# Kernel tuning notes

Measured on AMD Instinct MI355X. Metric: run time of the kernel, lower is better.

The kernel has to match this reference:

```python
import jax, jax.numpy as jnp
import numpy as np
import math

D_MODEL = 1024
N_HEAD = 16
D_HEAD = D_MODEL // N_HEAD
INIT_SIZE = 1200  # RelativeSinusoidalPositionalEmbedding init_size
SCALE = 1.0       # scale=False in __init__


def _rel_pos_embed(L, d_head):
    """Replicates RelativeSinusoidalPositionalEmbedding: table over positions
    [-601, 600] (num=init_size+1=1201 rows), padding row 0 zeroed, then gather
    rows for positions arange(-L/2, L/2) + origin_shift (origin_shift=601)."""
    num = INIT_SIZE + 1                      # 1201
    half = d_head // 2
    freq = jnp.exp(jnp.arange(half, dtype=jnp.float32) * (-math.log(10000.0) / (half - 1)))
    pos_vals = jnp.arange(-num // 2, num // 2, dtype=jnp.float32)   # -601..599 -> 1201 vals
    ang = pos_vals[:, None] * freq[None, :]
    table = jnp.concatenate([jnp.sin(ang), jnp.cos(ang)], axis=1)   # [num, d_head]
    table = table.at[0].set(0.0)             # padding_idx = 0
    origin_shift = num // 2 + 1              # 601
    idx = jnp.arange(-(L // 2), L // 2) + origin_shift   # L even -> L indices
    return table[idx]                        # [L, d_head]


def setup_inputs() -> dict:
    key = jax.random.key(0)
    k1, k2, k3, k4, k5 = jax.random.split(key, 5)
    B, L = 4, 1024
    embed = jax.random.normal(k1, (B, L, D_MODEL), dtype=jnp.float32)
    umask = jnp.ones((B, L), dtype=jnp.int32)                       # 1 = valid utterance
    qmask = jax.random.randint(k2, (B, L), 0, 2).astype(jnp.int64)  # speaker ids {0,1}
    W_qkv = jax.random.normal(k3, (D_MODEL, 4 * D_MODEL), dtype=jnp.float32) * 0.02
    W_pos = jax.random.normal(k4, (D_HEAD, 3 * D_MODEL), dtype=jnp.float32) * 0.02
    W_fc  = jax.random.normal(k5, (D_MODEL, D_MODEL), dtype=jnp.float32) * 0.02
    return {"embed": embed, "umask": umask, "qmask": qmask,
            "W_qkv": W_qkv, "W_pos": W_pos, "W_fc": W_fc}


def reference(embed, umask, qmask, W_qkv, W_pos, W_fc):
    B, L, d = embed.shape
    H, dh = N_HEAD, d // N_HEAD

    # qkv projection and head split
    q, k1, k2, v = jnp.split(embed @ W_qkv, 4, axis=-1)             # each [B, L, d]
    q  = q.reshape(B, L, H, dh).transpose(0, 2, 1, 3)               # [B, H, L, dh]
    k1 = k1.reshape(B, L, H, dh).transpose(0, 2, 1, 3)
    k2 = k2.reshape(B, L, H, dh).transpose(0, 2, 1, 3)
    v  = v.reshape(B, L, H, dh).transpose(0, 2, 1, 3)

    # relative position projections (detached sinusoids -> qk_pos linear)
    pe = _rel_pos_embed(L, dh)                                      # [L, dh]
    qp, kp1, kp2 = jnp.split(pe @ W_pos, 3, axis=-1)                # each [L, d]
    qp  = qp.reshape(L, H, dh).transpose(1, 0, 2)                   # [H, L, dh]
    kp1 = kp1.reshape(L, H, dh).transpose(1, 0, 2)
    kp2 = kp2.reshape(L, H, dh).transpose(1, 0, 2)

    pos1 = jnp.einsum('hqd,hkd->hqk', qp, kp1)                      # [H, L, L]
    pos2 = jnp.einsum('hqd,hkd->hqk', qp, kp2)

    attn_self  = jnp.einsum('bhqd,bhkd->bhqk', q, k1) + pos1[None]  # [B, H, L, L]
    attn_other = jnp.einsum('bhqd,bhkd->bhqk', q, k2) + pos2[None]

    # same-speaker mask: self-attn only where speakers match, other-attn where they differ
    qeq = (qmask[:, :, None] == qmask[:, None, :])                  # [B, L, L] bool
    attn_self  = jnp.where(qeq[:, None], attn_self, 0.0)
    attn_other = jnp.where(qeq[:, None], 0.0, attn_other)
    attn_add = (attn_self + attn_other) / SCALE

    # causal (order) mask + padding mask (eval-mode path of the module)
    order = jnp.triu(jnp.ones((L, L), dtype=bool), 1)[None] | (umask == 0)[:, None, :]
    attn = jnp.where(order[:, None], -jnp.inf, attn_add)
    p = jax.nn.softmax(attn, axis=-1)                               # dropout is identity in eval

    out = jnp.einsum('bhqk,bhkd->bhqd', p, v)                       # [B, H, L, dh]
    out = out.transpose(0, 2, 1, 3).reshape(B, L, d)
    return out @ W_fc
```

## Files before the change

### kernel.cpp

```cpp
#include <hip/hip_runtime.h>
#include <math.h>

#define NB 4
#define SEQ 1024
#define DMODEL 1024
#define NHEAD 16
#define DHEAD 64

typedef __attribute__((ext_vector_type(8))) short s16x8;
typedef __attribute__((ext_vector_type(4))) short s16x4;
typedef __attribute__((ext_vector_type(4))) float f32x4;

__device__ __forceinline__ short f2bf(float f) {
    union { float f; unsigned u; } x; x.f = f;
    unsigned r = x.u + 0x7fffu + ((x.u >> 16) & 1u);
    return (short)(r >> 16);
}

__device__ __forceinline__ unsigned cvtpk(float lo, float hi) {
    unsigned r;
    asm("v_cvt_pk_bf16_f32 %0, %1, %2" : "=v"(r) : "v"(lo), "v"(hi));
    return r;
}

__device__ __forceinline__ f32x4 mfma16(s16x8 a, s16x8 b, f32x4 c) {
    return __builtin_amdgcn_mfma_f32_16x16x32_bf16(a, b, c, 0, 0, 0);
}

__device__ __forceinline__ s16x8 cvt8(float4 a, float4 b) {
    s16x8 v;
    v[0] = f2bf(a.x); v[1] = f2bf(a.y); v[2] = f2bf(a.z); v[3] = f2bf(a.w);
    v[4] = f2bf(b.x); v[5] = f2bf(b.y); v[6] = f2bf(b.z); v[7] = f2bf(b.w);
    return v;
}

__device__ __forceinline__ s16x8 ldlds(const short* base, int byteoff) {
    return *(const s16x8*)((const char*)base + byteoff);
}

#define GLDS16(g, l) __builtin_amdgcn_global_load_lds( \
    (const __attribute__((address_space(1))) unsigned int*)(g), \
    (__attribute__((address_space(3))) unsigned int*)(l), 16, 0, 0)
#define GLDS4(g, l) __builtin_amdgcn_global_load_lds( \
    (const __attribute__((address_space(1))) unsigned int*)(g), \
    (__attribute__((address_space(3))) unsigned int*)(l), 4, 0, 0)

__global__ __launch_bounds__(256) void prep_kernel(
    const int* __restrict__ qmask, const int* __restrict__ umask,
    const float* __restrict__ Wpos, const float* __restrict__ embed,
    const float* __restrict__ Wqkv, const float* __restrict__ Wfc,
    int* __restrict__ PM, short* __restrict__ qpb,
    short* __restrict__ k1cat, short* __restrict__ k2cat,
    short* __restrict__ ebf, short* __restrict__ WqkvT,
    short* __restrict__ WfcT)
{
    __shared__ __align__(16) char smem[9216];
    int gbid = blockIdx.x;
    int tid = threadIdx.x;

    if (gbid < 4) {
        int b = gbid;
        for (int k = tid; k < 1088; k += 256) {
            int v = 2;
            if (k < 1024)
                v = (qmask[b * 1024 + k] & 1) | ((umask[b * 1024 + k] == 0) ? 2 : 0);
            PM[b * 1088 + k] = v;
        }
    } else if (gbid < 388) {
        int bid = gbid - 4;
        int s = bid >> 7;
        int l0 = (bid & 127) * 8;
        float (*pe)[64] = (float(*)[64])smem;

        for (int idx = tid; idx < 512; idx += 256) {
            int li = idx >> 6, t = idx & 63;
            float p = (float)(l0 + li - 512);
            int j = (t < 32) ? t : (t - 32);
            float f = expf(-0.2971077539f * (float)j);
            float a = p * f;
            pe[li][t] = (t < 32) ? sinf(a) : cosf(a);
        }
        __syncthreads();

        float acc[4][8] = {};
        const float* wp = Wpos + s * 1024 + tid;
        for (int t = 0; t < 64; ++t) {
            float w0 = wp[t * 3072];
            float w1 = wp[t * 3072 + 256];
            float w2 = wp[t * 3072 + 512];
            float w3 = wp[t * 3072 + 768];
            #pragma unroll
            for (int li = 0; li < 8; ++li) {
                float pv = pe[li][t];
                acc[0][li] += pv * w0; acc[1][li] += pv * w1;
                acc[2][li] += pv * w2; acc[3][li] += pv * w3;
            }
        }
        #pragma unroll
        for (int cc = 0; cc < 4; ++cc) {
            int c = tid + cc * 256;
            int h = c >> 6, d = c & 63;
            #pragma unroll
            for (int li = 0; li < 8; ++li) {
                short bv = f2bf(acc[cc][li]);
                if (s == 0) {
                    qpb[((size_t)(h << 10) + l0 + li) * 64 + d] = bv;
                } else {
                    short* dst = (s == 1) ? k1cat : k2cat;
                    #pragma unroll
                    for (int bb = 0; bb < 4; ++bb)
                        dst[((size_t)((bb * 16 + h) * 1024) + l0 + li) * 128 + 64 + d] = bv;
                }
            }
        }
    } else if (gbid < 2436) {
        int i = ((gbid - 388) * 256 + tid) * 8;
        float4 a = *(const float4*)(embed + i);
        float4 b = *(const float4*)(embed + i + 4);
        *(s16x8*)(ebf + i) = cvt8(a, b);
    } else {
        const float* W; short* WT; int N, bx, by;
        if (gbid < 3460) {
            int t = gbid - 2436;
            W = Wqkv; WT = WqkvT; N = 4096;
            bx = t & 63; by = t >> 6;
        } else {
            int t = gbid - 3460;
            W = Wfc; WT = WfcT; N = 1024;
            bx = t & 15; by = t >> 4;
        }
        short (*T)[72] = (short(*)[72])smem;
        int nt = bx * 64, kt = by * 64;
        int kl = tid >> 4;
        int nl = (tid & 15) * 4;
        #pragma unroll
        for (int rr = 0; rr < 4; ++rr) {
            int k = kl + rr * 16;
            float4 v = *(const float4*)(W + (size_t)(kt + k) * N + nt + nl);
            T[nl + 0][k] = f2bf(v.x);
            T[nl + 1][k] = f2bf(v.y);
            T[nl + 2][k] = f2bf(v.z);
            T[nl + 3][k] = f2bf(v.w);
        }
        __syncthreads();
        int nr = tid >> 2;
        int kc = (tid & 3) * 16;
        uint4 a = *(const uint4*)&T[nr][kc];
        uint4 b = *(const uint4*)&T[nr][kc + 8];
        short* dst = WT + (size_t)(nt + nr) * 1024 + kt + kc;
        *(uint4*)(dst) = a;
        *(uint4*)(dst + 8) = b;
    }
}

template<int EPI, int NCOLS>
__global__ __launch_bounds__(256) void gemm_nt(
    const short* __restrict__ A, const short* __restrict__ BT,
    short* __restrict__ o0, short* __restrict__ o1, short* __restrict__ o2,
    short* __restrict__ o3, float* __restrict__ of)
{
    __shared__ short As[2][128 * 32];
    __shared__ short Bs[2][128 * 32];

    int nwg = gridDim.x * gridDim.y;
    int lin = blockIdx.y * gridDim.x + blockIdx.x;
    int cpx = nwg >> 3;
    int swb = (lin & 7) * cpx + (lin >> 3);
    int bx = swb % gridDim.x, by = swb / gridDim.x;
    int m0 = by * 128, n0 = bx * 128;

    int tid = threadIdx.x;
    int w = tid >> 6, lane = tid & 63;
    int wm = w >> 1, wn = w & 1;
    int lq = lane & 15, lg = lane >> 4;

    f32x4 zero = {0.f, 0.f, 0.f, 0.f};
    f32x4 acc[4][4];
    #pragma unroll
    for (int i = 0; i < 4; ++i)
        #pragma unroll
        for (int j = 0; j < 4; ++j) acc[i][j] = zero;

    int swz = (((lane & 3) ^ ((lane >> 2) & 3)) << 3);
    int srow = lane >> 2;
    const short* aBase = A  + (size_t)(m0 + (w << 5) + srow) * 1024 + swz;
    const short* bBase = BT + (size_t)(n0 + (w << 5) + srow) * 1024 + swz;
    int dOff = w * 1024;

    GLDS16(aBase, &As[0][dOff]);
    GLDS16(aBase + 16 * 1024, &As[0][dOff + 512]);
    GLDS16(bBase, &Bs[0][dOff]);
    GLDS16(bBase + 16 * 1024, &Bs[0][dOff + 512]);

    int cur = 0;
    for (int kt = 0; kt < 1024; kt += 32) {
        if (kt + 32 < 1024) {
            int nxt = cur ^ 1;
            GLDS16(aBase + kt + 32, &As[nxt][dOff]);
            GLDS16(aBase + kt + 32 + 16 * 1024, &As[nxt][dOff + 512]);
            GLDS16(bBase + kt + 32, &Bs[nxt][dOff]);
            GLDS16(bBase + kt + 32 + 16 * 1024, &Bs[nxt][dOff + 512]);
            asm volatile("s_waitcnt vmcnt(4)" ::: "memory");
        } else {
            asm volatile("s_waitcnt vmcnt(0)" ::: "memory");
        }
        __builtin_amdgcn_s_barrier();
        asm volatile("" ::: "memory");

        s16x8 af[4], bfr[4];
        #pragma unroll
        for (int mt = 0; mt < 4; ++mt) {
            int row = wm * 64 + mt * 16 + lq;
            af[mt] = ldlds(As[cur], (row * 64 + lg * 16) ^ ((row & 3) << 4));
        }
        #pragma unroll
        for (int nt = 0; nt < 4; ++nt) {
            int row = wn * 64 + nt * 16 + lq;
            bfr[nt] = ldlds(Bs[cur], (row * 64 + lg * 16) ^ ((row & 3) << 4));
        }
        #pragma unroll
        for (int mt = 0; mt < 4; ++mt)
            #pragma unroll
            for (int nt = 0; nt < 4; ++nt)
                acc[mt][nt] = mfma16(af[mt], bfr[nt], acc[mt][nt]);

        asm volatile("" ::: "memory");
        __builtin_amdgcn_s_barrier();
        cur ^= 1;
    }

    #pragma unroll
    for (int nt = 0; nt < 4; ++nt) {
        int n = n0 + wn * 64 + nt * 16 + lq;
        int sec = n >> 10, hd = n & 1023;
        int hh = hd >> 6, d = hd & 63;
        #pragma unroll
        for (int mt = 0; mt < 4; ++mt) {
            int mb = m0 + wm * 64 + mt * 16 + lg * 4;
            if constexpr (EPI == 1) {
                #pragma unroll
                for (int r = 0; r < 4; ++r)
                    of[(size_t)(mb + r) * NCOLS + n] = acc[mt][nt][r];
            } else {
                int b = mb >> 10, li0 = mb & 1023;
                int bh = b * 16 + hh;
                if (sec == 3) {
                    s16x4 pv;
                    #pragma unroll
                    for (int r = 0; r < 4; ++r) pv[r] = f2bf(acc[mt][nt][r]);
                    *(s16x4*)(o3 + (((size_t)(bh * 64 + d)) << 10) + li0) = pv;
                } else {
                    #pragma unroll
                    for (int r = 0; r < 4; ++r) {
                        short bv = f2bf(acc[mt][nt][r]);
                        if (sec == 0)
                            o0[((size_t)(bh << 10) + li0 + r) * 64 + d] = bv;
                        else if (sec == 1)
                            o1[((size_t)bh * 1024 + li0 + r) * 128 + d] = bv;
                        else
                            o2[((size_t)bh * 1024 + li0 + r) * 128 + d] = bv;
                    }
                }
            }
        }
    }
}

__global__ __launch_bounds__(256) void attn_kernel(
    const short* __restrict__ qb, const short* __restrict__ k1cat,
    const short* __restrict__ k2cat, const short* __restrict__ vtb,
    const short* __restrict__ qpb, const int* __restrict__ PM,
    const int* __restrict__ qmask, short* __restrict__ ctx)
{
    __shared__ short K1s[2][32 * 128];
    __shared__ short K2s[2][32 * 128];
    __shared__ short Vs[2][64 * 32];
    __shared__ int   PMs[2][64];

    int bid = blockIdx.x;
    int xg = bid & 7, j = bid >> 3;
    int bh = xg * 8 + (j & 7);
    int qt = 15 - (j >> 3);
    int b = bh >> 4, h = bh & 15;

    int w = threadIdx.x >> 6, lane = threadIdx.x & 63;
    int lq = lane & 15, lg = lane >> 4;

    auto STAGE = [&](int d, int K0) {
        #pragma unroll
        for (int i = 0; i < 5; ++i) {
            int g = w * 5 + i;
            if (g < 8) {
                int row = g * 4 + (lane >> 4);
                int colb = ((lane & 15) << 4) ^ ((row & 7) << 4);
                const short* src = k1cat + ((size_t)bh * 1024 + K0 + row) * 128 + (colb >> 1);
                GLDS16(src, &K1s[d][g * 512]);
            } else if (g < 16) {
                int gg = g - 8;
                int row = gg * 4 + (lane >> 4);
                int colb = ((lane & 15) << 4) ^ ((row & 7) << 4);
                const short* src = k2cat + ((size_t)bh * 1024 + K0 + row) * 128 + (colb >> 1);
                GLDS16(src, &K2s[d][gg * 512]);
            } else {
                int c = g - 16;
                int row = c * 16 + (lane >> 2);
                int colb = ((lane & 3) << 4) ^ ((row & 3) << 4);
                const short* src = vtb + ((size_t)bh * 64 + row) * 1024 + K0 + (colb >> 1);
                GLDS16(src, &Vs[d][c * 512]);
            }
        }
        if (w == 0) {
            GLDS4(PM + b * 1088 + K0 + lane, &PMs[d][0]);
        }
    };

    f32x4 zero = {0.f, 0.f, 0.f, 0.f};

    int q0 = qt * 64 + w * 16;
    int q_glob = q0 + lq;

    const short* qrow  = qb  + ((size_t)bh * SEQ + q_glob) * DHEAD;
    const short* qprow = qpb + ((size_t)h  * SEQ + q_glob) * DHEAD;
    s16x8 qf0  = *(const s16x8*)(qrow + lg * 8);
    s16x8 qf1  = *(const s16x8*)(qrow + 32 + lg * 8);
    s16x8 qpf0 = *(const s16x8*)(qprow + lg * 8);
    s16x8 qpf1 = *(const s16x8*)(qprow + 32 + lg * 8);
    int qm_q = qmask[b * SEQ + q_glob] & 1;
    asm volatile("s_waitcnt vmcnt(0)" ::: "memory");

    f32x4 accO[4];
    #pragma unroll
    for (int i = 0; i < 4; ++i) accO[i] = zero;
    float m_run = -1e30f, l_run = 0.f;

    int nslab = 2 * qt + 2;
    STAGE(0, 0);

    #pragma unroll 1
    for (int t = 0; t < nslab; ++t) {
        int cur = t & 1;
        if (t + 1 < nslab) {
            STAGE(cur ^ 1, (t + 1) * 32);
            if (w == 0) asm volatile("s_waitcnt vmcnt(6)" ::: "memory");
            else        asm volatile("s_waitcnt vmcnt(5)" ::: "memory");
        } else {
            asm volatile("s_waitcnt vmcnt(0)" ::: "memory");
        }
        __builtin_amdgcn_s_barrier();
        asm volatile("" ::: "memory");

        int K0 = t * 32;
        if (K0 <= q0 + 15) {
            const short* b1 = K1s[cur];
            const short* b2 = K2s[cur];

            f32x4 s1v[2], s2v[2];
            __builtin_amdgcn_s_setprio(1);
            #pragma unroll
            for (int hh = 0; hh < 2; ++hh) {
                int row = hh * 16 + lq;
                int ro = row * 256 + (lg << 4);
                int sw = (row & 7) << 4;
                f32x4 tv = zero, uv = zero;
                tv = mfma16(ldlds(b1, (ro      ) ^ sw), qf0,  tv);
                tv = mfma16(ldlds(b1, (ro +  64) ^ sw), qf1,  tv);
                tv = mfma16(ldlds(b1, (ro + 128) ^ sw), qpf0, tv);
                tv = mfma16(ldlds(b1, (ro + 192) ^ sw), qpf1, tv);
                s1v[hh] = tv;
                uv = mfma16(ldlds(b2, (ro      ) ^ sw), qf0,  uv);
                uv = mfma16(ldlds(b2, (ro +  64) ^ sw), qf1,  uv);
                uv = mfma16(ldlds(b2, (ro + 128) ^ sw), qpf0, uv);
                uv = mfma16(ldlds(b2, (ro + 192) ^ sw), qpf1, uv);
                s2v[hh] = uv;
            }
            __builtin_amdgcn_s_setprio(0);

            int4 pmv0 = *(const int4*)&PMs[cur][lg * 4];
            int4 pmv1 = *(const int4*)&PMs[cur][16 + lg * 4];
            int pme[8] = {pmv0.x, pmv0.y, pmv0.z, pmv0.w,
                          pmv1.x, pmv1.y, pmv1.z, pmv1.w};

            float sv[8];
            #pragma unroll
            for (int i = 0; i < 8; ++i) {
                int hh = i >> 2, r = i & 3;
                int k_idx = K0 + hh * 16 + lg * 4 + r;
                int pm = pme[i];
                float s = ((pm & 1) == qm_q) ? s1v[hh][r] : s2v[hh][r];
                if (k_idx > q_glob || (pm & 2)) s = -INFINITY;
                sv[i] = s;
            }
            float tm = sv[0];
            #pragma unroll
            for (int i = 1; i < 8; ++i) tm = fmaxf(tm, sv[i]);
            tm = fmaxf(tm, __shfl_xor(tm, 16));
            tm = fmaxf(tm, __shfl_xor(tm, 32));

            if (!__all(tm <= m_run + 8.0f)) {
                float m_new = fmaxf(m_run, tm);
                float scale = __expf(m_run - m_new);
                m_run = m_new;
                l_run *= scale;
                f32x4 scv;
                scv[0] = __shfl(scale, lg * 4 + 0);
                scv[1] = __shfl(scale, lg * 4 + 1);
                scv[2] = __shfl(scale, lg * 4 + 2);
                scv[3] = __shfl(scale, lg * 4 + 3);
                #pragma unroll
                for (int dt = 0; dt < 4; ++dt) accO[dt] *= scv;
            }

            float p[8]; float ps = 0.f;
            #pragma unroll
            for (int i = 0; i < 8; ++i) { p[i] = __expf(sv[i] - m_run); ps += p[i]; }
            ps += __shfl_xor(ps, 16);
            ps += __shfl_xor(ps, 32);
            l_run += ps;

            unsigned dA0 = cvtpk(p[0], p[1]);
            unsigned dA1 = cvtpk(p[2], p[3]);
            unsigned dB0 = cvtpk(p[4], p[5]);
            unsigned dB1 = cvtpk(p[6], p[7]);
            int sl0 = lq + ((lg & 1) << 5);
            int sl1 = sl0 + 16;
            unsigned a0 = (unsigned)__shfl((int)dA0, sl0), a1 = (unsigned)__shfl((int)dA1, sl0);
            unsigned a2 = (unsigned)__shfl((int)dA0, sl1), a3 = (unsigned)__shfl((int)dA1, sl1);
            unsigned c0 = (unsigned)__shfl((int)dB0, sl0), c1 = (unsigned)__shfl((int)dB1, sl0);
            unsigned c2 = (unsigned)__shfl((int)dB0, sl1), c3 = (unsigned)__shfl((int)dB1, sl1);
            bool hi = (lg >= 2);
            union { unsigned u[4]; s16x8 v; } pa;
            pa.u[0] = hi ? c0 : a0; pa.u[1] = hi ? c1 : a1;
            pa.u[2] = hi ? c2 : a2; pa.u[3] = hi ? c3 : a3;

            __builtin_amdgcn_s_setprio(1);
            #pragma unroll
            for (int dt = 0; dt < 4; ++dt) {
                int vrow = dt * 16 + lq;
                int voff = (vrow * 64 + (lg << 4)) ^ ((vrow & 3) << 4);
                accO[dt] = mfma16(pa.v, ldlds(Vs[cur], voff), accO[dt]);
            }
            __builtin_amdgcn_s_setprio(0);
        }

        asm volatile("" ::: "memory");
        __builtin_amdgcn_s_barrier();
    }

    float inv = 1.0f / l_run;
    f32x4 invv;
    invv[0] = __shfl(inv, lg * 4 + 0);
    invv[1] = __shfl(inv, lg * 4 + 1);
    invv[2] = __shfl(inv, lg * 4 + 2);
    invv[3] = __shfl(inv, lg * 4 + 3);
    #pragma unroll
    for (int dt = 0; dt < 4; ++dt) {
        #pragma unroll
        for (int r = 0; r < 4; ++r) {
            int qo = q0 + lg * 4 + r;
            size_t off = ((size_t)(b * SEQ + qo)) * DMODEL + h * DHEAD + dt * 16 + lq;
            ctx[off] = f2bf(accO[dt][r] * invv[r]);
        }
    }
}

extern "C" void kernel_launch(void* const* d_in, const int* in_sizes, int n_in,
                              void* d_out, int out_size, void* d_ws, size_t ws_size,
                              hipStream_t stream) {
    const float* embed = (const float*)d_in[0];
    const int*   umask = (const int*)d_in[1];
    const int*   qmask = (const int*)d_in[2];
    const float* Wqkv  = (const float*)d_in[3];
    const float* Wpos  = (const float*)d_in[4];
    const float* Wfc   = (const float*)d_in[5];
    float* out = (float*)d_out;

    char* w = (char*)d_ws;
    short* qb    = (short*)(w + (0ull  << 20));
    short* vtb   = (short*)(w + (8ull  << 20));
    short* qpb   = (short*)(w + (16ull << 20));
    short* ctx   = (short*)(w + (18ull << 20));
    short* ebf   = ctx;
    short* k1cat = (short*)(w + (26ull << 20));
    short* k2cat = (short*)(w + (42ull << 20));
    int*   PM    = (int*)  (w + (58ull << 20));
    short* WqkvT = (short*)(w + (59ull << 20));
    short* WfcT  = (short*)(w + (67ull << 20));

    hipLaunchKernelGGL(prep_kernel, dim3(3716), dim3(256), 0, stream,
                       qmask, umask, Wpos, embed, Wqkv, Wfc,
                       PM, qpb, k1cat, k2cat, ebf, WqkvT, WfcT);
    hipLaunchKernelGGL((gemm_nt<0, 4096>), dim3(32, 32), dim3(256), 0, stream,
                       ebf, WqkvT, qb, k1cat, k2cat, vtb, (float*)nullptr);
    hipLaunchKernelGGL(attn_kernel, dim3(1024), dim3(256), 0, stream,
                       qb, k1cat, k2cat, vtb, qpb, PM, qmask, ctx);
    hipLaunchKernelGGL((gemm_nt<1, 1024>), dim3(8, 32), dim3(256), 0, stream,
                       ctx, WfcT, (short*)nullptr, (short*)nullptr, (short*)nullptr,
                       (short*)nullptr, out);
}
```

Measured before the change: 163.7 us.

## Triple-buffer GEMM K-loop and double attention query tile per workgroup

```diff
diff --git a/kernel.cpp b/kernel.cpp
--- a/kernel.cpp
+++ b/kernel.cpp
@@ -159,8 +159,8 @@
     short* __restrict__ o0, short* __restrict__ o1, short* __restrict__ o2,
     short* __restrict__ o3, float* __restrict__ of)
 {
-    __shared__ short As[2][128 * 32];
-    __shared__ short Bs[2][128 * 32];
+    __shared__ short As[3][128 * 32];
+    __shared__ short Bs[3][128 * 32];
 
     int nwg = gridDim.x * gridDim.y;
     int lin = blockIdx.y * gridDim.x + blockIdx.x;
@@ -187,19 +187,22 @@
     const short* bBase = BT + (size_t)(n0 + (w << 5) + srow) * 1024 + swz;
     int dOff = w * 1024;
 
-    GLDS16(aBase, &As[0][dOff]);
-    GLDS16(aBase + 16 * 1024, &As[0][dOff + 512]);
-    GLDS16(bBase, &Bs[0][dOff]);
-    GLDS16(bBase + 16 * 1024, &Bs[0][dOff + 512]);
-
-    int cur = 0;
+    #define STAGEG(D, KT) {                                       \
+        GLDS16(aBase + (KT), &As[D][dOff]);                       \
+        GLDS16(aBase + (KT) + 16 * 1024, &As[D][dOff + 512]);     \
+        GLDS16(bBase + (KT), &Bs[D][dOff]);                       \
+        GLDS16(bBase + (KT) + 16 * 1024, &Bs[D][dOff + 512]);     \
+    }
+
+    STAGEG(0, 0);
+    STAGEG(1, 32);
+
+    int cur = 0, stb = 2;
     for (int kt = 0; kt < 1024; kt += 32) {
-        if (kt + 32 < 1024) {
-            int nxt = cur ^ 1;
-            GLDS16(aBase + kt + 32, &As[nxt][dOff]);
-            GLDS16(aBase + kt + 32 + 16 * 1024, &As[nxt][dOff + 512]);
-            GLDS16(bBase + kt + 32, &Bs[nxt][dOff]);
-            GLDS16(bBase + kt + 32 + 16 * 1024, &Bs[nxt][dOff + 512]);
+        if (kt + 64 < 1024) {
+            STAGEG(stb, kt + 64);
+            asm volatile("s_waitcnt vmcnt(8)" ::: "memory");
+        } else if (kt + 32 < 1024) {
             asm volatile("s_waitcnt vmcnt(4)" ::: "memory");
         } else {
             asm volatile("s_waitcnt vmcnt(0)" ::: "memory");
@@ -226,8 +229,10 @@
 
         asm volatile("" ::: "memory");
         __builtin_amdgcn_s_barrier();
-        cur ^= 1;
+        cur = (cur == 2) ? 0 : cur + 1;
+        stb = (stb == 2) ? 0 : stb + 1;
     }
+    #undef STAGEG
 
     #pragma unroll
     for (int nt = 0; nt < 4; ++nt) {
@@ -266,7 +271,7 @@
     }
 }
 
-__global__ __launch_bounds__(256) void attn_kernel(
+__global__ __launch_bounds__(512) void attn_kernel(
     const short* __restrict__ qb, const short* __restrict__ k1cat,
     const short* __restrict__ k2cat, const short* __restrict__ vtb,
     const short* __restrict__ qpb, const int* __restrict__ PM,
@@ -280,7 +285,7 @@
     int bid = blockIdx.x;
     int xg = bid & 7, j = bid >> 3;
     int bh = xg * 8 + (j & 7);
-    int qt = 15 - (j >> 3);
+    int qt = 7 - (j >> 3);
     int b = bh >> 4, h = bh & 15;
 
     int w = threadIdx.x >> 6, lane = threadIdx.x & 63;
@@ -288,8 +293,8 @@
 
     auto STAGE = [&](int d, int K0) {
         #pragma unroll
-        for (int i = 0; i < 5; ++i) {
-            int g = w * 5 + i;
+        for (int i = 0; i < 3; ++i) {
+            int g = w + i * 8;
             if (g < 8) {
                 int row = g * 4 + (lane >> 4);
                 int colb = ((lane & 15) << 4) ^ ((row & 7) << 4);
@@ -301,7 +306,7 @@
                 int colb = ((lane & 15) << 4) ^ ((row & 7) << 4);
                 const short* src = k2cat + ((size_t)bh * 1024 + K0 + row) * 128 + (colb >> 1);
                 GLDS16(src, &K2s[d][gg * 512]);
-            } else {
+            } else if (g < 20) {
                 int c = g - 16;
                 int row = c * 16 + (lane >> 2);
                 int colb = ((lane & 3) << 4) ^ ((row & 3) << 4);
@@ -309,14 +314,14 @@
                 GLDS16(src, &Vs[d][c * 512]);
             }
         }
-        if (w == 0) {
+        if (w == 4) {
             GLDS4(PM + b * 1088 + K0 + lane, &PMs[d][0]);
         }
     };
 
     f32x4 zero = {0.f, 0.f, 0.f, 0.f};
 
-    int q0 = qt * 64 + w * 16;
+    int q0 = qt * 128 + w * 16;
     int q_glob = q0 + lq;
 
     const short* qrow  = qb  + ((size_t)bh * SEQ + q_glob) * DHEAD;
@@ -333,7 +338,7 @@
     for (int i = 0; i < 4; ++i) accO[i] = zero;
     float m_run = -1e30f, l_run = 0.f;
 
-    int nslab = 2 * qt + 2;
+    int nslab = 4 * qt + 4;
     STAGE(0, 0);
 
     #pragma unroll 1
@@ -341,8 +346,8 @@
         int cur = t & 1;
         if (t + 1 < nslab) {
             STAGE(cur ^ 1, (t + 1) * 32);
-            if (w == 0) asm volatile("s_waitcnt vmcnt(6)" ::: "memory");
-            else        asm volatile("s_waitcnt vmcnt(5)" ::: "memory");
+            if (w <= 4) asm volatile("s_waitcnt vmcnt(3)" ::: "memory");
+            else        asm volatile("s_waitcnt vmcnt(2)" ::: "memory");
         } else {
             asm volatile("s_waitcnt vmcnt(0)" ::: "memory");
         }
@@ -491,7 +496,7 @@
                        PM, qpb, k1cat, k2cat, ebf, WqkvT, WfcT);
     hipLaunchKernelGGL((gemm_nt<0, 4096>), dim3(32, 32), dim3(256), 0, stream,
                        ebf, WqkvT, qb, k1cat, k2cat, vtb, (float*)nullptr);
-    hipLaunchKernelGGL(attn_kernel, dim3(1024), dim3(256), 0, stream,
+    hipLaunchKernelGGL(attn_kernel, dim3(512), dim3(512), 0, stream,
                        qb, k1cat, k2cat, vtb, qpb, PM, qmask, ctx);
     hipLaunchKernelGGL((gemm_nt<1, 1024>), dim3(8, 32), dim3(256), 0, stream,
                        ctx, WfcT, (short*)nullptr, (short*)nullptr, (short*)nullptr,
```

Result: slower. 172.1 us (+5.1%).

## Move independent prep work into the QKV GEMM launch to overlap with it

Applied to the files above, without the earlier changes.

```diff
diff --git a/kernel.cpp b/kernel.cpp
--- a/kernel.cpp
+++ b/kernel.cpp
@@ -45,90 +45,23 @@
     (const __attribute__((address_space(1))) unsigned int*)(g), \
     (__attribute__((address_space(3))) unsigned int*)(l), 4, 0, 0)
 
-__global__ __launch_bounds__(256) void prep_kernel(
-    const int* __restrict__ qmask, const int* __restrict__ umask,
-    const float* __restrict__ Wpos, const float* __restrict__ embed,
-    const float* __restrict__ Wqkv, const float* __restrict__ Wfc,
-    int* __restrict__ PM, short* __restrict__ qpb,
-    short* __restrict__ k1cat, short* __restrict__ k2cat,
-    short* __restrict__ ebf, short* __restrict__ WqkvT,
-    short* __restrict__ WfcT)
+__global__ __launch_bounds__(256) void prep_a_kernel(
+    const float* __restrict__ embed, const float* __restrict__ Wqkv,
+    short* __restrict__ ebf, short* __restrict__ WqkvT)
 {
     __shared__ __align__(16) char smem[9216];
-    int gbid = blockIdx.x;
+    int gb = blockIdx.x;
     int tid = threadIdx.x;
 
-    if (gbid < 4) {
-        int b = gbid;
-        for (int k = tid; k < 1088; k += 256) {
-            int v = 2;
-            if (k < 1024)
-                v = (qmask[b * 1024 + k] & 1) | ((umask[b * 1024 + k] == 0) ? 2 : 0);
-            PM[b * 1088 + k] = v;
-        }
-    } else if (gbid < 388) {
-        int bid = gbid - 4;
-        int s = bid >> 7;
-        int l0 = (bid & 127) * 8;
-        float (*pe)[64] = (float(*)[64])smem;
-
-        for (int idx = tid; idx < 512; idx += 256) {
-            int li = idx >> 6, t = idx & 63;
-            float p = (float)(l0 + li - 512);
-            int j = (t < 32) ? t : (t - 32);
-            float f = expf(-0.2971077539f * (float)j);
-            float a = p * f;
-            pe[li][t] = (t < 32) ? sinf(a) : cosf(a);
-        }
-        __syncthreads();
-
-        float acc[4][8] = {};
-        const float* wp = Wpos + s * 1024 + tid;
-        for (int t = 0; t < 64; ++t) {
-            float w0 = wp[t * 3072];
-            float w1 = wp[t * 3072 + 256];
-            float w2 = wp[t * 3072 + 512];
-            float w3 = wp[t * 3072 + 768];
-            #pragma unroll
-            for (int li = 0; li < 8; ++li) {
-                float pv = pe[li][t];
-                acc[0][li] += pv * w0; acc[1][li] += pv * w1;
-                acc[2][li] += pv * w2; acc[3][li] += pv * w3;
-            }
-        }
-        #pragma unroll
-        for (int cc = 0; cc < 4; ++cc) {
-            int c = tid + cc * 256;
-            int h = c >> 6, d = c & 63;
-            #pragma unroll
-            for (int li = 0; li < 8; ++li) {
-                short bv = f2bf(acc[cc][li]);
-                if (s == 0) {
-                    qpb[((size_t)(h << 10) + l0 + li) * 64 + d] = bv;
-                } else {
-                    short* dst = (s == 1) ? k1cat : k2cat;
-                    #pragma unroll
-                    for (int bb = 0; bb < 4; ++bb)
-                        dst[((size_t)((bb * 16 + h) * 1024) + l0 + li) * 128 + 64 + d] = bv;
-                }
-            }
-        }
-    } else if (gbid < 2436) {
-        int i = ((gbid - 388) * 256 + tid) * 8;
+    if (gb < 2048) {
+        int i = (gb * 256 + tid) * 8;
         float4 a = *(const float4*)(embed + i);
         float4 b = *(const float4*)(embed + i + 4);
         *(s16x8*)(ebf + i) = cvt8(a, b);
     } else {
-        const float* W; short* WT; int N, bx, by;
-        if (gbid < 3460) {
-            int t = gbid - 2436;
-            W = Wqkv; WT = WqkvT; N = 4096;
-            bx = t & 63; by = t >> 6;
-        } else {
-            int t = gbid - 3460;
-            W = Wfc; WT = WfcT; N = 1024;
-            bx = t & 15; by = t >> 4;
-        }
+        int t = gb - 2048;
+        int bx = t & 63, by = t >> 6;
+        const int N = 4096;
         short (*T)[72] = (short(*)[72])smem;
         int nt = bx * 64, kt = by * 64;
         int kl = tid >> 4;
@@ -136,7 +69,7 @@
         #pragma unroll
         for (int rr = 0; rr < 4; ++rr) {
             int k = kl + rr * 16;
-            float4 v = *(const float4*)(W + (size_t)(kt + k) * N + nt + nl);
+            float4 v = *(const float4*)(Wqkv + (size_t)(kt + k) * N + nt + nl);
             T[nl + 0][k] = f2bf(v.x);
             T[nl + 1][k] = f2bf(v.y);
             T[nl + 2][k] = f2bf(v.z);
@@ -147,29 +80,118 @@
         int kc = (tid & 3) * 16;
         uint4 a = *(const uint4*)&T[nr][kc];
         uint4 b = *(const uint4*)&T[nr][kc + 8];
-        short* dst = WT + (size_t)(nt + nr) * 1024 + kt + kc;
+        short* dst = WqkvT + (size_t)(nt + nr) * 1024 + kt + kc;
         *(uint4*)(dst) = a;
         *(uint4*)(dst + 8) = b;
     }
 }
 
-template<int EPI, int NCOLS>
-__global__ __launch_bounds__(256) void gemm_nt(
+__global__ __launch_bounds__(256) void gemm_qkv_fused(
     const short* __restrict__ A, const short* __restrict__ BT,
     short* __restrict__ o0, short* __restrict__ o1, short* __restrict__ o2,
-    short* __restrict__ o3, float* __restrict__ of)
+    short* __restrict__ o3,
+    const int* __restrict__ qmask, const int* __restrict__ umask,
+    const float* __restrict__ Wpos, const float* __restrict__ Wfc,
+    int* __restrict__ PM, short* __restrict__ qpb, short* __restrict__ WfcT)
 {
     __shared__ short As[2][128 * 32];
     __shared__ short Bs[2][128 * 32];
 
-    int nwg = gridDim.x * gridDim.y;
-    int lin = blockIdx.y * gridDim.x + blockIdx.x;
-    int cpx = nwg >> 3;
+    int gb = blockIdx.x;
+    int tid = threadIdx.x;
+
+    if (gb < 644) {
+        char* smem = (char*)&As[0][0];
+        if (gb < 4) {
+            int b = gb;
+            for (int k = tid; k < 1088; k += 256) {
+                int v = 2;
+                if (k < 1024)
+                    v = (qmask[b * 1024 + k] & 1) | ((umask[b * 1024 + k] == 0) ? 2 : 0);
+                PM[b * 1088 + k] = v;
+            }
+        } else if (gb < 388) {
+            int bid = gb - 4;
+            int s = bid >> 7;
+            int l0 = (bid & 127) * 8;
+            float (*pe)[64] = (float(*)[64])smem;
+
+            for (int idx = tid; idx < 512; idx += 256) {
+                int li = idx >> 6, t = idx & 63;
+                float p = (float)(l0 + li - 512);
+                int j = (t < 32) ? t : (t - 32);
+                float f = expf(-0.2971077539f * (float)j);
+                float a = p * f;
+                pe[li][t] = (t < 32) ? sinf(a) : cosf(a);
+            }
+            __syncthreads();
+
+            float acc[4][8] = {};
+            const float* wp = Wpos + s * 1024 + tid;
+            for (int t = 0; t < 64; ++t) {
+                float w0 = wp[t * 3072];
+                float w1 = wp[t * 3072 + 256];
+                float w2 = wp[t * 3072 + 512];
+                float w3 = wp[t * 3072 + 768];
+                #pragma unroll
+                for (int li = 0; li < 8; ++li) {
+                    float pv = pe[li][t];
+                    acc[0][li] += pv * w0; acc[1][li] += pv * w1;
+                    acc[2][li] += pv * w2; acc[3][li] += pv * w3;
+                }
+            }
+            #pragma unroll
+            for (int cc = 0; cc < 4; ++cc) {
+                int c = tid + cc * 256;
+                int h = c >> 6, d = c & 63;
+                #pragma unroll
+                for (int li = 0; li < 8; ++li) {
+                    short bv = f2bf(acc[cc][li]);
+                    if (s == 0) {
+                        qpb[((size_t)(h << 10) + l0 + li) * 64 + d] = bv;
+                    } else {
+                        short* dst = (s == 1) ? o1 : o2;
+                        #pragma unroll
+                        for (int bb = 0; bb < 4; ++bb)
+                            dst[((size_t)((bb * 16 + h) * 1024) + l0 + li) * 128 + 64 + d] = bv;
+                    }
+                }
+            }
+        } else {
+            int t = gb - 388;
+            int bx = t & 15, by = t >> 4;
+            const int N = 1024;
+            short (*T)[72] = (short(*)[72])smem;
+            int nt = bx * 64, kt = by * 64;
+            int kl = tid >> 4;
+            int nl = (tid & 15) * 4;
+            #pragma unroll
+            for (int rr = 0; rr < 4; ++rr) {
+                int k = kl + rr * 16;
+                float4 v = *(const float4*)(Wfc + (size_t)(kt + k) * N + nt + nl);
+                T[nl + 0][k] = f2bf(v.x);
+                T[nl + 1][k] = f2bf(v.y);
+                T[nl + 2][k] = f2bf(v.z);
+                T[nl + 3][k] = f2bf(v.w);
+            }
+            __syncthreads();
+            int nr = tid >> 2;
+            int kc = (tid & 3) * 16;
+            uint4 a = *(const uint4*)&T[nr][kc];
+            uint4 b = *(const uint4*)&T[nr][kc + 8];
+            short* dst = WfcT + (size_t)(nt + nr) * 1024 + kt + kc;
+            *(uint4*)(dst) = a;
+            *(uint4*)(dst + 8) = b;
+        }
+        return;
+    }
+
+    int lin = gb - 644;
+    int cpx = 1024 >> 3;
     int swb = (lin & 7) * cpx + (lin >> 3);
-    int bx = swb % gridDim.x, by = swb / gridDim.x;
+    int bx = swb & 31, by = swb >> 5;
     int m0 = by * 128, n0 = bx * 128;
 
-    int tid = threadIdx.x;
     int w = tid >> 6, lane = tid & 63;
     int wm = w >> 1, wn = w & 1;
     int lq = lane & 15, lg = lane >> 4;
@@ -237,31 +259,113 @@
         #pragma unroll
         for (int mt = 0; mt < 4; ++mt) {
             int mb = m0 + wm * 64 + mt * 16 + lg * 4;
-            if constexpr (EPI == 1) {
+            int b = mb >> 10, li0 = mb & 1023;
+            int bh = b * 16 + hh;
+            if (sec == 3) {
+                s16x4 pv;
                 #pragma unroll
-                for (int r = 0; r < 4; ++r)
-                    of[(size_t)(mb + r) * NCOLS + n] = acc[mt][nt][r];
+                for (int r = 0; r < 4; ++r) pv[r] = f2bf(acc[mt][nt][r]);
+                *(s16x4*)(o3 + (((size_t)(bh * 64 + d)) << 10) + li0) = pv;
             } else {
-                int b = mb >> 10, li0 = mb & 1023;
-                int bh = b * 16 + hh;
-                if (sec == 3) {
-                    s16x4 pv;
-                    #pragma unroll
-                    for (int r = 0; r < 4; ++r) pv[r] = f2bf(acc[mt][nt][r]);
-                    *(s16x4*)(o3 + (((size_t)(bh * 64 + d)) << 10) + li0) = pv;
-                } else {
-                    #pragma unroll
-                    for (int r = 0; r < 4; ++r) {
-                        short bv = f2bf(acc[mt][nt][r]);
-                        if (sec == 0)
-                            o0[((size_t)(bh << 10) + li0 + r) * 64 + d] = bv;
-                        else if (sec == 1)
-                            o1[((size_t)bh * 1024 + li0 + r) * 128 + d] = bv;
-                        else
-                            o2[((size_t)bh * 1024 + li0 + r) * 128 + d] = bv;
-                    }
+                #pragma unroll
+                for (int r = 0; r < 4; ++r) {
+                    short bv = f2bf(acc[mt][nt][r]);
+                    if (sec == 0)
+                        o0[((size_t)(bh << 10) + li0 + r) * 64 + d] = bv;
+                    else if (sec == 1)
+                        o1[((size_t)bh * 1024 + li0 + r) * 128 + d] = bv;
+                    else
+                        o2[((size_t)bh * 1024 + li0 + r) * 128 + d] = bv;
                 }
             }
+        }
+    }
+}
+
+template<int EPI, int NCOLS>
+__global__ __launch_bounds__(256) void gemm_nt(
+    const short* __restrict__ A, const short* __restrict__ BT,
+    float* __restrict__ of)
+{
+    __shared__ short As[2][128 * 32];
+    __shared__ short Bs[2][128 * 32];
+
+    int nwg = gridDim.x * gridDim.y;
+    int lin = blockIdx.y * gridDim.x + blockIdx.x;
+    int cpx = nwg >> 3;
+    int swb = (lin & 7) * cpx + (lin >> 3);
+    int bx = swb % gridDim.x, by = swb / gridDim.x;
+    int m0 = by * 128, n0 = bx * 128;
+
+    int tid = threadIdx.x;
+    int w = tid >> 6, lane = tid & 63;
+    int wm = w >> 1, wn = w & 1;
+    int lq = lane & 15, lg = lane >> 4;
+
+    f32x4 zero = {0.f, 0.f, 0.f, 0.f};
+    f32x4 acc[4][4];
+    #pragma unroll
+    for (int i = 0; i < 4; ++i)
+        #pragma unroll
+        for (int j = 0; j < 4; ++j) acc[i][j] = zero;
+
+    int swz = (((lane & 3) ^ ((lane >> 2) & 3)) << 3);
+    int srow = lane >> 2;
+    const short* aBase = A  + (size_t)(m0 + (w << 5) + srow) * 1024 + swz;
+    const short* bBase = BT + (size_t)(n0 + (w << 5) + srow) * 1024 + swz;
+    int dOff = w * 1024;
+
+    GLDS16(aBase, &As[0][dOff]);
+    GLDS16(aBase + 16 * 1024, &As[0][dOff + 512]);
+    GLDS16(bBase, &Bs[0][dOff]);
+    GLDS16(bBase + 16 * 1024, &Bs[0][dOff + 512]);
+
+    int cur = 0;
+    for (int kt = 0; kt < 1024; kt += 32) {
+        if (kt + 32 < 1024) {
+            int nxt = cur ^ 1;
+            GLDS16(aBase + kt + 32, &As[nxt][dOff]);
+            GLDS16(aBase + kt + 32 + 16 * 1024, &As[nxt][dOff + 512]);
+            GLDS16(bBase + kt + 32, &Bs[nxt][dOff]);
+            GLDS16(bBase + kt + 32 + 16 * 1024, &Bs[nxt][dOff + 512]);
+            asm volatile("s_waitcnt vmcnt(4)" ::: "memory");
+        } else {
+            asm volatile("s_waitcnt vmcnt(0)" ::: "memory");
+        }
+        __builtin_amdgcn_s_barrier();
+        asm volatile("" ::: "memory");
+
+        s16x8 af[4], bfr[4];
+        #pragma unroll
+        for (int mt = 0; mt < 4; ++mt) {
+            int row = wm * 64 + mt * 16 + lq;
+            af[mt] = ldlds(As[cur], (row * 64 + lg * 16) ^ ((row & 3) << 4));
+        }
+        #pragma unroll
+        for (int nt = 0; nt < 4; ++nt) {
+            int row = wn * 64 + nt * 16 + lq;
+            bfr[nt] = ldlds(Bs[cur], (row * 64 + lg * 16) ^ ((row & 3) << 4));
+        }
+        #pragma unroll
+        for (int mt = 0; mt < 4; ++mt)
+            #pragma unroll
+            for (int nt = 0; nt < 4; ++nt)
+                acc[mt][nt] = mfma16(af[mt], bfr[nt], acc[mt][nt]);
+
+        asm volatile("" ::: "memory");
+        __builtin_amdgcn_s_barrier();
+        cur ^= 1;
+    }
+
+    #pragma unroll
+    for (int nt = 0; nt < 4; ++nt) {
+        int n = n0 + wn * 64 + nt * 16 + lq;
+        #pragma unroll
+        for (int mt = 0; mt < 4; ++mt) {
+            int mb = m0 + wm * 64 + mt * 16 + lg * 4;
+            #pragma unroll
+            for (int r = 0; r < 4; ++r)
+                of[(size_t)(mb + r) * NCOLS + n] = acc[mt][nt][r];
         }
     }
 }
@@ -486,14 +590,13 @@
     short* WqkvT = (short*)(w + (59ull << 20));
     short* WfcT  = (short*)(w + (67ull << 20));
 
-    hipLaunchKernelGGL(prep_kernel, dim3(3716), dim3(256), 0, stream,
-                       qmask, umask, Wpos, embed, Wqkv, Wfc,
-                       PM, qpb, k1cat, k2cat, ebf, WqkvT, WfcT);
-    hipLaunchKernelGGL((gemm_nt<0, 4096>), dim3(32, 32), dim3(256), 0, stream,
-                       ebf, WqkvT, qb, k1cat, k2cat, vtb, (float*)nullptr);
+    hipLaunchKernelGGL(prep_a_kernel, dim3(3072), dim3(256), 0, stream,
+                       embed, Wqkv, ebf, WqkvT);
+    hipLaunchKernelGGL(gemm_qkv_fused, dim3(1668), dim3(256), 0, stream,
+                       ebf, WqkvT, qb, k1cat, k2cat, vtb,
+                       qmask, umask, Wpos, Wfc, PM, qpb, WfcT);
     hipLaunchKernelGGL(attn_kernel, dim3(1024), dim3(256), 0, stream,
                        qb, k1cat, k2cat, vtb, qpb, PM, qmask, ctx);
     hipLaunchKernelGGL((gemm_nt<1, 1024>), dim3(8, 32), dim3(256), 0, stream,
-                       ctx, WfcT, (short*)nullptr, (short*)nullptr, (short*)nullptr,
-                       (short*)nullptr, out);
-}
+                       ctx, WfcT, out);
+}
```

Result: no change. 162.3 us (-0.8%).
